# Kernel optimization log

Hardware: AMD Instinct MI355X
Metric: run time of the kernel (lower is better)

Reference implementation:

```python
import jax, jax.numpy as jnp
import numpy as np

SCALE = 1.0 / np.sqrt(256.0)  # 1/sqrt(hidden_dim)


def setup_inputs() -> dict:
    key = jax.random.key(0)
    ks = jax.random.split(key, 9)
    N, C, H, W = 32, 256, 32, 32
    D, T = 256, 512
    s = lambda k, shape, fan: jax.random.normal(k, shape, jnp.float32) / np.sqrt(fan)
    return {
        "x": jax.random.normal(ks[0], (N, C, H, W), jnp.float32),
        "t": jax.random.normal(ks[1], (N, T), jnp.float32),
        "W_t": s(ks[2], (C, T), T),
        "b_t": jnp.zeros((C,), jnp.float32),
        "Wq": s(ks[3], (D, C), C),
        "Wk": s(ks[4], (D, C), C),
        "Wv": s(ks[5], (D, C), C),
        "Wp": s(ks[6], (C, D), D),
        "bp": jnp.zeros((C,), jnp.float32),
    }


def reference(x, t, W_t, b_t, Wq, Wk, Wv, Wp, bp):
    N, C, H, W = x.shape
    h = x
    # time embedding: Linear + ReLU, broadcast over spatial dims
    temb = jax.nn.relu(t @ W_t.T + b_t)  # [N, C]
    x = x + temb[:, :, None, None]
    # transpose(1,3): [N, C, H, W] -> [N, W, H, C]
    xc = jnp.transpose(x, (0, 3, 2, 1))
    q = xc @ Wq.T  # [N, W, H, D]
    k = xc @ Wk.T
    v = xc @ Wv.T
    # full spatial attention scores: [N, W, H, w, h]
    qk = jnp.einsum('NWHd,Nwhd->NWHwh', q, k) * SCALE
    qk = jax.nn.softmax(qk.reshape(N, W, H, W * H), axis=-1)
    qk = qk.reshape(N, W, H, W, H)
    out = jnp.einsum('NWHwh,Nwhd->NWHd', qk, v)  # [N, W, H, D]
    out = out @ Wp.T + bp  # [N, W, H, C]
    out = jnp.transpose(out, (0, 3, 2, 1))  # [N, C, H, W]
    return out + h
```

## Files before the change

### kernel.cpp

```cpp
#include <hip/hip_runtime.h>
#include <hip/hip_bf16.h>

#define NB 32
#define CD 256
#define SS 1024
#define DD 256
#define TT 512
#define QSCALE 0.09016844f

typedef __attribute__((ext_vector_type(8))) short s16x8;
typedef __attribute__((ext_vector_type(4))) short s16x4;
typedef __attribute__((ext_vector_type(4))) float f32x4;
typedef __attribute__((ext_vector_type(16))) float f32x16;

__device__ __forceinline__ unsigned short f2bf(float f) {
  unsigned u = __builtin_bit_cast(unsigned, f);
  u = (u + 0x7FFFu + ((u >> 16) & 1u)) >> 16;
  return (unsigned short)u;
}
__device__ __forceinline__ float bf2f(unsigned short h) {
  return __builtin_bit_cast(float, ((unsigned)h) << 16);
}
__device__ __forceinline__ unsigned pk2(float a, float b) {
  float2 f2; f2.x = a; f2.y = b;
  __hip_bfloat162 h = __float22bfloat162_rn(f2);
  unsigned u;
  __builtin_memcpy(&u, &h, 4);
  return u;
}
#define GLOAD16(gp, lp)                                                        \
  __builtin_amdgcn_global_load_lds(                                            \
      (const __attribute__((address_space(1))) unsigned int*)(const void*)(gp),\
      (__attribute__((address_space(3))) unsigned int*)(void*)(lp), 16, 0, 0)

__global__ __launch_bounds__(256) void k_misc(const float* __restrict__ t,
    const float* __restrict__ Wt, const float* __restrict__ bt, float* __restrict__ temb,
    const float* __restrict__ wq, const float* __restrict__ wk,
    const float* __restrict__ wv, const float* __restrict__ wp,
    unsigned short* __restrict__ dst) {
  const int b = blockIdx.x;
  if (b < 1024) {
    const int i = b * 256 + threadIdx.x;
    const int which = i >> 16, off = i & 65535;
    const float* s = which == 0 ? wq : which == 1 ? wk : which == 2 ? wv : wp;
    dst[i] = f2bf(s[off]);
  } else {
    const int n = b - 1024, c = threadIdx.x;
    const float4* tv = (const float4*)(t + (size_t)n * TT);
    const float4* wvv = (const float4*)(Wt + (size_t)c * TT);
    float acc = 0.f;
#pragma unroll 8
    for (int i = 0; i < TT / 4; ++i) {
      float4 a = tv[i], bb = wvv[i];
      acc += a.x * bb.x + a.y * bb.y + a.z * bb.z + a.w * bb.w;
    }
    acc += bt[c];
    temb[n * CD + c] = fmaxf(acc, 0.f);
  }
}

__global__ __launch_bounds__(256) void k_addT(const float* __restrict__ x,
    const float* __restrict__ temb, unsigned short* __restrict__ xb) {
  __shared__ float tile[32][33];
  const int tx = threadIdx.x & 31, ty = threadIdx.x >> 5;
  const int n = blockIdx.z, s0 = blockIdx.y * 32, c0 = blockIdx.x * 32;
#pragma unroll
  for (int i = 0; i < 4; ++i) {
    const int cc = ty + i * 8;
    tile[cc][tx] = x[((size_t)n * CD + c0 + cc) * SS + s0 + tx] + temb[n * CD + c0 + cc];
  }
  __syncthreads();
  unsigned short* op = xb + ((size_t)n * SS + s0) * CD + c0;
#pragma unroll
  for (int i = 0; i < 4; ++i) {
    const int ss = ty + i * 8;
    op[(size_t)ss * CD + tx] = f2bf(tile[tx][ss]);
  }
}

__global__ __launch_bounds__(256) void k_qkv(const unsigned short* __restrict__ A,
    const unsigned short* __restrict__ wb, unsigned short* __restrict__ qb,
    unsigned short* __restrict__ kb, unsigned short* __restrict__ vtb) {
  __shared__ __attribute__((aligned(16))) unsigned short As[128 * 32];
  __shared__ __attribute__((aligned(16))) unsigned short Bs[128 * 32];
  const int which = blockIdx.z >> 5, n = blockIdx.z & 31;
  const int s0 = blockIdx.x * 128;
  const int d0 = blockIdx.y * 128;
  const unsigned short* B = wb + which * 65536;
  const int tid = threadIdx.x;
  const int lane = tid & 63, wid = tid >> 6;
  const int lo = lane & 15, hi = lane >> 4;
  const int wr = wid >> 1, wc = wid & 1;
  const unsigned short* An = A + (size_t)n * SS * CD;
  f32x4 acc[4][4] = {};
  for (int k0 = 0; k0 < CD; k0 += 32) {
#pragma unroll
    for (int i = 0; i < 2; ++i) {
      const int seg = i * 256 + wid * 64 + lane;
      const int row = seg >> 2, c8 = seg & 3;
      GLOAD16(An + (size_t)(s0 + row) * CD + k0 + c8 * 8, As + (size_t)(i * 256 + wid * 64) * 8);
      GLOAD16(B + (size_t)(d0 + row) * CD + k0 + c8 * 8, Bs + (size_t)(i * 256 + wid * 64) * 8);
    }
    __syncthreads();
    s16x8 a[4], b[4];
#pragma unroll
    for (int mi = 0; mi < 4; ++mi)
      a[mi] = *(const s16x8*)&As[(wr * 64 + mi * 16 + lo) * 32 + hi * 8];
#pragma unroll
    for (int ni = 0; ni < 4; ++ni)
      b[ni] = *(const s16x8*)&Bs[(wc * 64 + ni * 16 + lo) * 32 + hi * 8];
#pragma unroll
    for (int mi = 0; mi < 4; ++mi)
#pragma unroll
      for (int ni = 0; ni < 4; ++ni)
        acc[mi][ni] = __builtin_amdgcn_mfma_f32_16x16x32_bf16(a[mi], b[ni], acc[mi][ni], 0, 0, 0);
    __syncthreads();
  }
  if (which < 2) {
    const float osc = which == 0 ? QSCALE : 1.0f;
    unsigned short* On = (which == 0 ? qb : kb) + (size_t)n * SS * DD;
#pragma unroll
    for (int mi = 0; mi < 4; ++mi) {
      const int r0 = s0 + wr * 64 + mi * 16 + hi * 4;
#pragma unroll
      for (int ni = 0; ni < 4; ++ni) {
        const int col = d0 + wc * 64 + ni * 16 + lo;
#pragma unroll
        for (int r = 0; r < 4; ++r)
          On[(size_t)(r0 + r) * DD + col] = f2bf(acc[mi][ni][r] * osc);
      }
    }
  } else {
    unsigned short* On = vtb + (size_t)n * DD * SS;
#pragma unroll
    for (int mi = 0; mi < 4; ++mi) {
      const int r0 = s0 + wr * 64 + mi * 16 + hi * 4;
#pragma unroll
      for (int ni = 0; ni < 4; ++ni) {
        const int col = d0 + wc * 64 + ni * 16 + lo;
        s16x4 v;
#pragma unroll
        for (int r = 0; r < 4; ++r) v[r] = (short)f2bf(acc[mi][ni][r]);
        *(s16x4*)&On[(size_t)col * SS + r0] = v;
      }
    }
  }
}

__global__ __launch_bounds__(256, 2) void k_attn(const unsigned short* __restrict__ qb,
    const unsigned short* __restrict__ kb, const unsigned short* __restrict__ vtb,
    unsigned short* __restrict__ ob) {
  __shared__ __attribute__((aligned(16))) unsigned short lds[29696];
  const int bid = blockIdx.x;
  const int xcd = bid & 7, inner = bid >> 3;
  const int n = xcd + ((inner >> 4) << 3);
  const int sub = inner & 15;
  const int qt = sub & 7, dh = sub >> 3;
  const int tid = threadIdx.x, lane = tid & 63, w = tid >> 6;
  const int l31 = lane & 31, h = lane >> 5;
  const int dblk = dh * 128;
  const unsigned short* Kn = kb + (size_t)n * SS * DD;
  const unsigned short* Vn = vtb + ((size_t)n * DD + dblk) * SS;
  unsigned short* Pw = lds + 24576 + w * 1280;
  const int qrow = qt * 128 + w * 32 + l31;

  const unsigned short* Qp = qb + ((size_t)n * SS + qrow) * DD + h * 8;
  s16x8 qf[16];
#pragma unroll
  for (int ks = 0; ks < 16; ++ks) qf[ks] = *(const s16x8*)(Qp + ks * 16);

  f32x16 acc[4] = {};
  float mrun = -3.0e38f, lrun = 0.f;

  auto STAGE = [&](int buf, int jt) {
    const int j0 = jt * 32;
    unsigned short* KsB = lds + buf * 8192;
    unsigned short* VsB = lds + 16384 + buf * 4096;
#pragma unroll
    for (int i = 0; i < 4; ++i) {
      const int idx = i * 256 + w * 64 + lane;
      const int row = idx >> 5, c8 = idx & 31;
      GLOAD16(Kn + (size_t)(j0 + row) * DD + ((c8 ^ (row & 7)) << 3),
              KsB + (size_t)(i * 256 + w * 64) * 8);
    }
#pragma unroll
    for (int i = 0; i < 2; ++i) {
      const int idx = i * 256 + w * 64 + lane;
      const int row = idx >> 2, c8 = idx & 3;
      GLOAD16(Vn + (size_t)row * SS + j0 + ((c8 ^ ((row >> 1) & 3)) << 3),
              VsB + (size_t)(i * 256 + w * 64) * 8);
    }
  };

  STAGE(0, 0);
  __syncthreads();

  int cur = 0;
#pragma unroll 1
  for (int jt = 0; jt < 32; ++jt) {
    if (jt + 1 < 32) STAGE(cur ^ 1, jt + 1);
    const unsigned short* Ks = lds + cur * 8192;
    const unsigned short* Vs = lds + 16384 + cur * 4096;
    f32x16 sc = {};
    __builtin_amdgcn_s_setprio(1);
#pragma unroll
    for (int ks = 0; ks < 16; ++ks) {
      const s16x8 kf = *(const s16x8*)&Ks[l31 * 256 + ((((ks * 2 + h)) ^ (l31 & 7)) << 3)];
      sc = __builtin_amdgcn_mfma_f32_32x32x16_bf16(kf, qf[ks], sc, 0, 0, 0);
    }
    __builtin_amdgcn_s_setprio(0);
    float pm = sc[0];
#pragma unroll
    for (int i = 1; i < 16; ++i) pm = fmaxf(pm, sc[i]);
    pm = fmaxf(pm, __shfl_xor(pm, 32, 64));
    if (__any(pm > mrun + 8.f)) {
      const float mn = fmaxf(mrun, pm);
      const float corr = exp2f(mrun - mn);
      mrun = mn; lrun *= corr;
#pragma unroll
      for (int dc = 0; dc < 4; ++dc)
#pragma unroll
        for (int i = 0; i < 16; ++i) acc[dc][i] *= corr;
    }
#pragma unroll
    for (int i = 0; i < 16; ++i) sc[i] = exp2f(sc[i] - mrun);
    lrun += (((sc[0] + sc[1]) + (sc[2] + sc[3])) + ((sc[4] + sc[5]) + (sc[6] + sc[7]))) +
            (((sc[8] + sc[9]) + (sc[10] + sc[11])) + ((sc[12] + sc[13]) + (sc[14] + sc[15])));
#pragma unroll
    for (int t = 0; t < 4; ++t) {
      uint2 u;
      u.x = pk2(sc[t * 4 + 0], sc[t * 4 + 1]);
      u.y = pk2(sc[t * 4 + 2], sc[t * 4 + 3]);
      *(uint2*)&Pw[l31 * 40 + t * 8 + h * 4] = u;
    }
    const s16x8 pa0 = *(const s16x8*)&Pw[l31 * 40 + h * 8];
    const s16x8 pa1 = *(const s16x8*)&Pw[l31 * 40 + 16 + h * 8];
    __builtin_amdgcn_s_setprio(1);
#pragma unroll
    for (int dc = 0; dc < 4; ++dc) {
      const s16x8 vf0 = *(const s16x8*)&Vs[(dc * 32 + l31) * 32 + ((h ^ ((l31 >> 1) & 3)) << 3)];
      acc[dc] = __builtin_amdgcn_mfma_f32_32x32x16_bf16(vf0, pa0, acc[dc], 0, 0, 0);
    }
#pragma unroll
    for (int dc = 0; dc < 4; ++dc) {
      const s16x8 vf1 = *(const s16x8*)&Vs[(dc * 32 + l31) * 32 + (((2 + h) ^ ((l31 >> 1) & 3)) << 3)];
      acc[dc] = __builtin_amdgcn_mfma_f32_32x32x16_bf16(vf1, pa1, acc[dc], 0, 0, 0);
    }
    __builtin_amdgcn_s_setprio(0);
    __syncthreads();
    cur ^= 1;
  }
  lrun += __shfl_xor(lrun, 32, 64);
  const float inv = 1.0f / lrun;
  unsigned short* Op = ob + ((size_t)n * SS + qrow) * DD + dblk;
#pragma unroll
  for (int dc = 0; dc < 4; ++dc)
#pragma unroll
    for (int rg = 0; rg < 4; ++rg) {
      uint2 u;
      u.x = pk2(acc[dc][rg * 4 + 0] * inv, acc[dc][rg * 4 + 1] * inv);
      u.y = pk2(acc[dc][rg * 4 + 2] * inv, acc[dc][rg * 4 + 3] * inv);
      *(uint2*)(Op + dc * 32 + rg * 8 + h * 4) = u;
    }
}

__global__ __launch_bounds__(256) void k_proj(const unsigned short* __restrict__ ob,
    const unsigned short* __restrict__ wpb, const float* __restrict__ bp,
    const float* __restrict__ x, float* __restrict__ out) {
  __shared__ __attribute__((aligned(16))) unsigned short As[128 * 32];
  __shared__ __attribute__((aligned(16))) unsigned short Bs[128 * 32];
  const int n = blockIdx.z;
  const int s0 = blockIdx.x * 128;
  const int c0 = blockIdx.y * 128;
  const int tid = threadIdx.x;
  const int lane = tid & 63, wid = tid >> 6;
  const int lo = lane & 15, hi = lane >> 4;
  const int wr = wid >> 1, wc = wid & 1;
  const unsigned short* On = ob + (size_t)n * SS * DD;
  f32x4 acc[4][4] = {};
  for (int k0 = 0; k0 < DD; k0 += 32) {
#pragma unroll
    for (int i = 0; i < 2; ++i) {
      const int seg = i * 256 + wid * 64 + lane;
      const int row = seg >> 2, c8 = seg & 3;
      GLOAD16(wpb + (size_t)(c0 + row) * DD + k0 + c8 * 8, As + (size_t)(i * 256 + wid * 64) * 8);
      GLOAD16(On + (size_t)(s0 + row) * DD + k0 + c8 * 8, Bs + (size_t)(i * 256 + wid * 64) * 8);
    }
    __syncthreads();
    s16x8 a[4], b[4];
#pragma unroll
    for (int mi = 0; mi < 4; ++mi)
      a[mi] = *(const s16x8*)&As[(wr * 64 + mi * 16 + lo) * 32 + hi * 8];
#pragma unroll
    for (int ni = 0; ni < 4; ++ni)
      b[ni] = *(const s16x8*)&Bs[(wc * 64 + ni * 16 + lo) * 32 + hi * 8];
#pragma unroll
    for (int mi = 0; mi < 4; ++mi)
#pragma unroll
      for (int ni = 0; ni < 4; ++ni)
        acc[mi][ni] = __builtin_amdgcn_mfma_f32_16x16x32_bf16(a[mi], b[ni], acc[mi][ni], 0, 0, 0);
    __syncthreads();
  }
#pragma unroll
  for (int mi = 0; mi < 4; ++mi) {
#pragma unroll
    for (int r = 0; r < 4; ++r) {
      const int c = c0 + wr * 64 + mi * 16 + hi * 4 + r;
      const float bpc = bp[c];
      const size_t base = ((size_t)n * CD + c) * SS;
#pragma unroll
      for (int ni = 0; ni < 4; ++ni) {
        const int s = s0 + wc * 64 + ni * 16 + lo;
        out[base + s] = acc[mi][ni][r] + bpc + x[base + s];
      }
    }
  }
}

extern "C" void kernel_launch(void* const* d_in, const int* in_sizes, int n_in,
                              void* d_out, int out_size, void* d_ws, size_t ws_size,
                              hipStream_t stream) {
  const float* x  = (const float*)d_in[0];
  const float* t  = (const float*)d_in[1];
  const float* Wt = (const float*)d_in[2];
  const float* bt = (const float*)d_in[3];
  const float* Wq = (const float*)d_in[4];
  const float* Wk = (const float*)d_in[5];
  const float* Wv = (const float*)d_in[6];
  const float* Wp = (const float*)d_in[7];
  const float* bp = (const float*)d_in[8];
  char* ws = (char*)d_ws;
  float* temb        = (float*)ws;
  unsigned short* wb = (unsigned short*)(ws + 32768);
  unsigned short* xb = (unsigned short*)(ws + 557056);
  unsigned short* qb = (unsigned short*)(ws + 17334272);
  unsigned short* kb = (unsigned short*)(ws + 34111488);
  unsigned short* vtb = (unsigned short*)(ws + 50888704);
  unsigned short* ob = (unsigned short*)(ws + 67665920);
  float* out = (float*)d_out;

  k_misc<<<1056, 256, 0, stream>>>(t, Wt, bt, temb, Wq, Wk, Wv, Wp, wb);
  k_addT<<<dim3(8, 32, 32), 256, 0, stream>>>(x, temb, xb);
  k_qkv<<<dim3(8, 2, 96), 256, 0, stream>>>(xb, wb, qb, kb, vtb);
  k_attn<<<512, 256, 0, stream>>>(qb, kb, vtb, ob);
  k_proj<<<dim3(8, 2, 32), 256, 0, stream>>>(ob, wb + 196608, bp, x, out);
}
```

Measured before the change: 145.5 us.

## Replace LDS P round-trip with permlane32 swaps and raise attention occupancy

The attention kernel no longer writes the softmax probabilities to a per-wave LDS scratch and reads them back as MFMA operands. It now packs them to bf16 in registers and rearranges them across half-waves with permlane32_swap. The cross-half max and sum reductions also use permlane32_swap instead of shfl_xor. Dropping the scratch shrinks LDS from about 58KB to 48KB, and the launch bound rises to 3 blocks per CU for higher occupancy, at the risk of register spills under the tighter VGPR budget.

Measured after the change: 189.5 us. 1.3x slower.

```diff
diff --git a/kernel.cpp b/kernel.cpp
--- a/kernel.cpp
+++ b/kernel.cpp
@@ -12,6 +12,7 @@
 typedef __attribute__((ext_vector_type(4))) short s16x4;
 typedef __attribute__((ext_vector_type(4))) float f32x4;
 typedef __attribute__((ext_vector_type(16))) float f32x16;
+typedef __attribute__((ext_vector_type(4))) unsigned int u32x4;
 
 __device__ __forceinline__ unsigned short f2bf(float f) {
   unsigned u = __builtin_bit_cast(unsigned, f);
@@ -27,6 +28,9 @@
   unsigned u;
   __builtin_memcpy(&u, &h, 4);
   return u;
+}
+__device__ __forceinline__ float asf(unsigned u) {
+  return __builtin_bit_cast(float, u);
 }
 #define GLOAD16(gp, lp)                                                        \
   __builtin_amdgcn_global_load_lds(                                            \
@@ -147,10 +151,10 @@
   }
 }
 
-__global__ __launch_bounds__(256, 2) void k_attn(const unsigned short* __restrict__ qb,
+__global__ __launch_bounds__(256, 3) void k_attn(const unsigned short* __restrict__ qb,
     const unsigned short* __restrict__ kb, const unsigned short* __restrict__ vtb,
     unsigned short* __restrict__ ob) {
-  __shared__ __attribute__((aligned(16))) unsigned short lds[29696];
+  __shared__ __attribute__((aligned(16))) unsigned short lds[24576];
   const int bid = blockIdx.x;
   const int xcd = bid & 7, inner = bid >> 3;
   const int n = xcd + ((inner >> 4) << 3);
@@ -161,7 +165,6 @@
   const int dblk = dh * 128;
   const unsigned short* Kn = kb + (size_t)n * SS * DD;
   const unsigned short* Vn = vtb + ((size_t)n * DD + dblk) * SS;
-  unsigned short* Pw = lds + 24576 + w * 1280;
   const int qrow = qt * 128 + w * 32 + l31;
 
   const unsigned short* Qp = qb + ((size_t)n * SS + qrow) * DD + h * 8;
@@ -209,10 +212,15 @@
       sc = __builtin_amdgcn_mfma_f32_32x32x16_bf16(kf, qf[ks], sc, 0, 0, 0);
     }
     __builtin_amdgcn_s_setprio(0);
-    float pm = sc[0];
-#pragma unroll
-    for (int i = 1; i < 16; ++i) pm = fmaxf(pm, sc[i]);
-    pm = fmaxf(pm, __shfl_xor(pm, 32, 64));
+    float pm = fmaxf(fmaxf(fmaxf(sc[0], sc[1]), fmaxf(sc[2], sc[3])),
+                     fmaxf(fmaxf(sc[4], sc[5]), fmaxf(sc[6], sc[7])));
+    pm = fmaxf(pm, fmaxf(fmaxf(fmaxf(sc[8], sc[9]), fmaxf(sc[10], sc[11])),
+                         fmaxf(fmaxf(sc[12], sc[13]), fmaxf(sc[14], sc[15]))));
+    {
+      auto rp = __builtin_amdgcn_permlane32_swap(__builtin_bit_cast(unsigned, pm),
+                                                 __builtin_bit_cast(unsigned, pm), false, false);
+      pm = fmaxf(asf(rp[0]), asf(rp[1]));
+    }
     if (__any(pm > mrun + 8.f)) {
       const float mn = fmaxf(mrun, pm);
       const float corr = exp2f(mrun - mn);
@@ -226,15 +234,18 @@
     for (int i = 0; i < 16; ++i) sc[i] = exp2f(sc[i] - mrun);
     lrun += (((sc[0] + sc[1]) + (sc[2] + sc[3])) + ((sc[4] + sc[5]) + (sc[6] + sc[7]))) +
             (((sc[8] + sc[9]) + (sc[10] + sc[11])) + ((sc[12] + sc[13]) + (sc[14] + sc[15])));
-#pragma unroll
-    for (int t = 0; t < 4; ++t) {
-      uint2 u;
-      u.x = pk2(sc[t * 4 + 0], sc[t * 4 + 1]);
-      u.y = pk2(sc[t * 4 + 2], sc[t * 4 + 3]);
-      *(uint2*)&Pw[l31 * 40 + t * 8 + h * 4] = u;
-    }
-    const s16x8 pa0 = *(const s16x8*)&Pw[l31 * 40 + h * 8];
-    const s16x8 pa1 = *(const s16x8*)&Pw[l31 * 40 + 16 + h * 8];
+    const unsigned wv0 = pk2(sc[0], sc[1]),   wv1 = pk2(sc[2], sc[3]);
+    const unsigned wv2 = pk2(sc[4], sc[5]),   wv3 = pk2(sc[6], sc[7]);
+    const unsigned wv4 = pk2(sc[8], sc[9]),   wv5 = pk2(sc[10], sc[11]);
+    const unsigned wv6 = pk2(sc[12], sc[13]), wv7 = pk2(sc[14], sc[15]);
+    auto r02 = __builtin_amdgcn_permlane32_swap(wv0, wv2, false, false);
+    auto r13 = __builtin_amdgcn_permlane32_swap(wv1, wv3, false, false);
+    auto r46 = __builtin_amdgcn_permlane32_swap(wv4, wv6, false, false);
+    auto r57 = __builtin_amdgcn_permlane32_swap(wv5, wv7, false, false);
+    const u32x4 pa0u = {r02[0], r13[0], r02[1], r13[1]};
+    const u32x4 pa1u = {r46[0], r57[0], r46[1], r57[1]};
+    const s16x8 pa0 = __builtin_bit_cast(s16x8, pa0u);
+    const s16x8 pa1 = __builtin_bit_cast(s16x8, pa1u);
     __builtin_amdgcn_s_setprio(1);
 #pragma unroll
     for (int dc = 0; dc < 4; ++dc) {
@@ -250,7 +261,11 @@
     __syncthreads();
     cur ^= 1;
   }
-  lrun += __shfl_xor(lrun, 32, 64);
+  {
+    auto rl = __builtin_amdgcn_permlane32_swap(__builtin_bit_cast(unsigned, lrun),
+                                               __builtin_bit_cast(unsigned, lrun), false, false);
+    lrun = asf(rl[0]) + asf(rl[1]);
+  }
   const float inv = 1.0f / lrun;
   unsigned short* Op = ob + ((size_t)n * SS + qrow) * DD + dblk;
 #pragma unroll
```
